# Optimization experiments

Hardware: AMD Instinct MI355X
Metric: run time of the kernel (lower is better)

## Reference

```python
import jax, jax.numpy as jnp
import numpy as np

B, S, D = 32, 1024, 256
F_, K = 256, 3
T = 8192
LN_EPS = 1e-5


def _conv1d(x, w, b, padding):
    # x: [B, S, C_in], w: [C_out, C_in, K] -> [B, S, C_out]
    y = jax.lax.conv_general_dilated(
        x.transpose(0, 2, 1), w, window_strides=(1,),
        padding=[(padding, padding)], dimension_numbers=('NCH', 'OIH', 'NCH'))
    return y.transpose(0, 2, 1) + b


def _layernorm(x, g, b):
    mu = jnp.mean(x, axis=-1, keepdims=True)
    var = jnp.mean(jnp.square(x - mu), axis=-1, keepdims=True)
    return (x - mu) * jax.lax.rsqrt(var + LN_EPS) * g + b


def setup_inputs() -> dict:
    key = jax.random.key(0)
    ks = jax.random.split(key, 8)
    sc = 0.02
    return {
        'x': jax.random.normal(ks[0], (B, S, D), dtype=jnp.float32),
        'mask': jnp.zeros((B, S), dtype=bool),
        'duration': jax.random.randint(ks[1], (B, S), 0, 8, dtype=jnp.int32),
        'max_len': T,
        'conv1_w': jax.random.normal(ks[2], (F_, D, K), dtype=jnp.float32) * sc,
        'conv1_b': jnp.zeros((F_,), dtype=jnp.float32),
        'ln1_g': jnp.ones((F_,), dtype=jnp.float32),
        'ln1_b': jnp.zeros((F_,), dtype=jnp.float32),
        'conv2_w': jax.random.normal(ks[3], (F_, F_, K), dtype=jnp.float32) * sc,
        'conv2_b': jnp.zeros((F_,), dtype=jnp.float32),
        'ln2_g': jnp.ones((F_,), dtype=jnp.float32),
        'ln2_b': jnp.zeros((F_,), dtype=jnp.float32),
        'lin_w': jax.random.normal(ks[4], (F_, 1), dtype=jnp.float32) * sc,
        'lin_b': jnp.zeros((1,), dtype=jnp.float32),
    }


def reference(x, mask, duration, max_len, conv1_w, conv1_b, ln1_g, ln1_b,
              conv2_w, conv2_b, ln2_g, ln2_b, lin_w, lin_b):
    # ---- duration predictor (eval mode: dropout = identity) ----
    h = _conv1d(x, conv1_w, conv1_b, (K - 1) // 2)
    h = _layernorm(jax.nn.relu(h), ln1_g, ln1_b)
    h = _conv1d(h, conv2_w, conv2_b, 1)
    h = _layernorm(jax.nn.relu(h), ln2_g, ln2_b)
    log_dur = (h @ lin_w + lin_b)[..., 0]  # [B, S]
    log_dur = jnp.where(mask, 0.0, log_dur)

    # ---- length regulator: repeat_interleave + pad, done as one gather ----
    dur = duration.astype(jnp.int32)
    cum = jnp.cumsum(dur, axis=1)                                   # [B, S]
    t = jnp.arange(max_len, dtype=jnp.int32)                        # [T]
    src_idx = jax.vmap(lambda c: jnp.searchsorted(c, t, side='right'))(cum)  # [B, T]
    mel_len = jnp.minimum(cum[:, -1], max_len)                      # [B]
    valid = t[None, :] < mel_len[:, None]                           # [B, T]
    src_idx = jnp.clip(src_idx, 0, x.shape[1] - 1)
    out = jnp.take_along_axis(x, src_idx[:, :, None], axis=1)       # [B, T, D]
    out = jnp.where(valid[:, :, None], out, 0.0)
    # duration_target path -> duration_rounded = duration, mel_mask stays None
    return out, log_dur, dur, mel_len
```

## Files before the change

kernel.cpp:

```cpp
#include <hip/hip_runtime.h>
#include <cstddef>

constexpr int Bb   = 32;
constexpr int Ss   = 1024;
constexpr int Dd   = 256;
constexpr int Ff   = 256;
constexpr int TMAX = 8192;
constexpr int MM   = Bb * Ss;
constexpr int KK   = 768;
constexpr int SP   = 1026;
constexpr float LN_EPS = 1e-5f;
constexpr int PIT  = 72;
constexpr int OPIT = 264;

constexpr int GEMM_BLK  = MM / 64;
constexpr int RIDER_PER = 2048;
constexpr int RIDER_F4  = 4096;

typedef __bf16 bf16x8 __attribute__((ext_vector_type(8)));
typedef __bf16 bf16x4 __attribute__((ext_vector_type(4)));
typedef float  f32x4  __attribute__((ext_vector_type(4)));

__global__ __launch_bounds__(256) void prep_k(
    const float* __restrict__ w1, const float* __restrict__ w2,
    __bf16* __restrict__ wTT1, __bf16* __restrict__ wTT2,
    const int* __restrict__ dur, float* __restrict__ dur_out,
    float* __restrict__ mel_out, int* __restrict__ idx,
    __bf16* __restrict__ xp2)
{
    __shared__ int ic[1024];
    __shared__ int sc[256];
    const int blk = blockIdx.x;
    const int tid = threadIdx.x;

    if (blk < 1536) {
        int i = blk * 256 + tid;
        const float* w = w1;
        __bf16* o = wTT1;
        int j = i;
        if (j >= Ff * KK) { j -= Ff * KK; w = w2; o = wTT2; }
        int d  = j & 255;
        int fk = j >> 8;
        int f  = fk / 3;
        int k  = fk - f * 3;
        o[(size_t)f * KK + k * 256 + d] = (__bf16)w[((size_t)(f * 256 + d)) * 3 + k];
        return;
    }
    if (blk >= 1568) {
        int j = (blk - 1568) * 256 + tid;
        int b = j >> 7;
        int r = (j >> 6) & 1;
        int d = (j & 63) * 4;
        *(bf16x4*)&xp2[((size_t)b * SP + (size_t)r * (SP - 1)) * 256 + d] =
            (bf16x4)(__bf16)0.f;
        return;
    }
    int b = blk - 1536;
    int4 d4 = ((const int4*)(dur + b * 1024))[tid];
    int l0 = d4.x, l1 = l0 + d4.y, l2 = l1 + d4.z, l3 = l2 + d4.w;
    sc[tid] = l3;
    __syncthreads();
    for (int off = 1; off < 256; off <<= 1) {
        int v = (tid >= off) ? sc[tid - off] : 0;
        __syncthreads();
        sc[tid] += v;
        __syncthreads();
    }
    int excl = sc[tid] - l3;
    ((int4*)ic)[tid] = make_int4(excl + l0, excl + l1, excl + l2, excl + l3);
    ((float4*)(dur_out + b * 1024))[tid] =
        make_float4((float)d4.x, (float)d4.y, (float)d4.z, (float)d4.w);
    if (tid == 255) mel_out[b] = (float)min(excl + l3, TMAX);
    __syncthreads();
    int mel = min(ic[1023], TMAX);
    for (int t = tid; t < TMAX; t += 256) {
        int lo = 0, hi = 1024;
        #pragma unroll
        for (int it = 0; it < 10; ++it) {
            int mid = (lo + hi) >> 1;
            if (ic[mid] <= t) lo = mid + 1; else hi = mid;
        }
        idx[b * TMAX + t] = (t < mel) ? min(lo, 1023) : -1;
    }
}

template<int MODE>
__global__ __launch_bounds__(256, 3) void gemm_fused(
    const float* __restrict__ Xf,
    const __bf16* __restrict__ Ap,
    const __bf16* __restrict__ Bw,
    const float* __restrict__ bias,
    const float* __restrict__ g, const float* __restrict__ bt,
    const float* __restrict__ lw, const float* __restrict__ lb,
    const unsigned char* __restrict__ mask,
    __bf16* __restrict__ outB, float* __restrict__ outF,
    const int* __restrict__ idx, f32x4* __restrict__ outv)
{
    __shared__ __bf16 As[64 * PIT];
    __shared__ __bf16 Bs[64 * OPIT];
    __shared__ __bf16 Bs2[256 * PIT - 64 * OPIT];

    const int tid = threadIdx.x;

    if (blockIdx.x >= GEMM_BLK) {
        int rblk = blockIdx.x - GEMM_BLK + MODE * RIDER_PER;
        size_t base = (size_t)rblk * RIDER_F4 + tid;
        int sarr[16];
        #pragma unroll
        for (int it = 0; it < 16; ++it) {
            size_t gg = base + (size_t)it * 256;
            sarr[it] = idx[gg >> 6];
        }
        f32x4 v[16];
        #pragma unroll
        for (int it = 0; it < 16; ++it) {
            size_t gg = base + (size_t)it * 256;
            int row = (int)(gg >> 6);
            int col = (int)(gg & 63);
            v[it] = (f32x4)0.f;
            if (sarr[it] >= 0) {
                int b = row >> 13;
                v[it] = ((const f32x4*)Xf)[((size_t)(b << 10) + sarr[it]) * 64 + col];
            }
        }
        #pragma unroll
        for (int it = 0; it < 16; ++it)
            __builtin_nontemporal_store(v[it], &outv[base + (size_t)it * 256]);
        return;
    }

    const int m0   = blockIdx.x * 64;
    const int bb   = m0 >> 10;
    const int s0   = m0 & 1023;
    const int wave = tid >> 6;
    const int lane = tid & 63;
    const int wn   = wave * 64;
    const int lm   = lane & 15;
    const int lk   = lane >> 4;

    __bf16* BsK = Bs;

    f32x4 acc[4][4] = {};

    for (int step = 0; step < KK / 64; ++step) {
        const int kk0  = step * 64;
        const int kblk = kk0 >> 8;
        const int d0   = kk0 & 255;

        if constexpr (MODE == 0) {
            #pragma unroll
            for (int i = 0; i < 4; ++i) {
                int c = i * 256 + tid;
                int r = c >> 4, q = c & 15;
                int sg = s0 + r + kblk - 1;
                bf16x4 o = (bf16x4)(__bf16)0.f;
                if ((unsigned)sg < 1024u) {
                    float4 v = *(const float4*)&Xf[
                        (((size_t)(bb << 10) + sg) << 8) + d0 + q * 4];
                    o[0] = (__bf16)v.x; o[1] = (__bf16)v.y;
                    o[2] = (__bf16)v.z; o[3] = (__bf16)v.w;
                }
                *(bf16x4*)&As[r * PIT + q * 4] = o;
            }
        } else {
            const __bf16* aSrc = Ap + (((size_t)(bb * SP + s0 + kblk)) << 8) + d0;
            #pragma unroll
            for (int i = 0; i < 2; ++i) {
                int c = i * 256 + tid, r = c >> 3, q = c & 7;
                *(bf16x8*)&As[r * PIT + q * 8] =
                    *(const bf16x8*)&aSrc[((size_t)r << 8) + q * 8];
            }
        }
        const __bf16* bSrc = Bw + kk0;
        #pragma unroll
        for (int i = 0; i < 8; ++i) {
            int c = i * 256 + tid, r = c >> 3, q = c & 7;
            *(bf16x8*)&BsK[r * PIT + q * 8] =
                *(const bf16x8*)&bSrc[(size_t)r * KK + q * 8];
        }
        __syncthreads();
        #pragma unroll
        for (int kc = 0; kc < 2; ++kc) {
            bf16x8 af[4], bfr[4];
            #pragma unroll
            for (int mi = 0; mi < 4; ++mi)
                af[mi] = *(const bf16x8*)&As[(mi * 16 + lm) * PIT + kc * 32 + lk * 8];
            #pragma unroll
            for (int ni = 0; ni < 4; ++ni)
                bfr[ni] = *(const bf16x8*)&BsK[(wn + ni * 16 + lm) * PIT + kc * 32 + lk * 8];
            #pragma unroll
            for (int mi = 0; mi < 4; ++mi)
                #pragma unroll
                for (int ni = 0; ni < 4; ++ni)
                    acc[mi][ni] = __builtin_amdgcn_mfma_f32_16x16x32_bf16(
                        af[mi], bfr[ni], acc[mi][ni], 0, 0, 0);
        }
        __syncthreads();
    }

    float* scrS = (float*)As;
    float* scrQ = scrS + 256;

    float s_[4][4] = {}, q_[4][4] = {};
    #pragma unroll
    for (int ni = 0; ni < 4; ++ni) {
        float bv = bias[wn + ni * 16 + lm];
        #pragma unroll
        for (int mi = 0; mi < 4; ++mi)
            #pragma unroll
            for (int r = 0; r < 4; ++r) {
                float h = fmaxf(acc[mi][ni][r] + bv, 0.f);
                acc[mi][ni][r] = h;
                s_[mi][r] += h;
                q_[mi][r] += h * h;
            }
    }
    #pragma unroll
    for (int off = 1; off < 16; off <<= 1)
        #pragma unroll
        for (int mi = 0; mi < 4; ++mi)
            #pragma unroll
            for (int r = 0; r < 4; ++r) {
                s_[mi][r] += __shfl_xor(s_[mi][r], off, 64);
                q_[mi][r] += __shfl_xor(q_[mi][r], off, 64);
            }
    if (lm == 0) {
        #pragma unroll
        for (int mi = 0; mi < 4; ++mi)
            #pragma unroll
            for (int r = 0; r < 4; ++r) {
                int row = mi * 16 + lk * 4 + r;
                scrS[wave * 64 + row] = s_[mi][r];
                scrQ[wave * 64 + row] = q_[mi][r];
            }
    }
    __syncthreads();

    float mu[4][4], rs[4][4];
    #pragma unroll
    for (int mi = 0; mi < 4; ++mi)
        #pragma unroll
        for (int r = 0; r < 4; ++r) {
            int row = mi * 16 + lk * 4 + r;
            float S = scrS[row] + scrS[64 + row] + scrS[128 + row] + scrS[192 + row];
            float Q = scrQ[row] + scrQ[64 + row] + scrQ[128 + row] + scrQ[192 + row];
            float m_ = S * (1.f / 256.f);
            float v_ = Q * (1.f / 256.f) - m_ * m_;
            mu[mi][r] = m_;
            rs[mi][r] = rsqrtf(v_ + LN_EPS);
        }

    if constexpr (MODE == 0) {
        __bf16* tile = Bs;
        #pragma unroll
        for (int ni = 0; ni < 4; ++ni) {
            int col = wn + ni * 16 + lm;
            float gv = g[col], bv2 = bt[col];
            #pragma unroll
            for (int mi = 0; mi < 4; ++mi)
                #pragma unroll
                for (int r = 0; r < 4; ++r) {
                    int row = mi * 16 + lk * 4 + r;
                    float o = (acc[mi][ni][r] - mu[mi][r]) * rs[mi][r] * gv + bv2;
                    tile[row * OPIT + col] = (__bf16)o;
                }
        }
        __syncthreads();
        size_t obase = ((size_t)(bb * SP + s0 + 1)) << 8;
        #pragma unroll
        for (int i = 0; i < 8; ++i) {
            int c = i * 256 + tid;
            int row = c >> 5, q = c & 31;
            *(bf16x8*)&outB[obase + ((size_t)row << 8) + q * 8] =
                *(bf16x8*)&tile[row * OPIT + q * 8];
        }
    } else {
        float p_[4][4] = {};
        #pragma unroll
        for (int ni = 0; ni < 4; ++ni) {
            int col = wn + ni * 16 + lm;
            float gv = g[col], bv2 = bt[col], wv = lw[col];
            #pragma unroll
            for (int mi = 0; mi < 4; ++mi)
                #pragma unroll
                for (int r = 0; r < 4; ++r) {
                    float o = (acc[mi][ni][r] - mu[mi][r]) * rs[mi][r] * gv + bv2;
                    p_[mi][r] += o * wv;
                }
        }
        #pragma unroll
        for (int off = 1; off < 16; off <<= 1)
            #pragma unroll
            for (int mi = 0; mi < 4; ++mi)
                #pragma unroll
                for (int r = 0; r < 4; ++r)
                    p_[mi][r] += __shfl_xor(p_[mi][r], off, 64);
        __syncthreads();
        if (lm == 0) {
            #pragma unroll
            for (int mi = 0; mi < 4; ++mi)
                #pragma unroll
                for (int r = 0; r < 4; ++r)
                    scrS[wave * 64 + (mi * 16 + lk * 4 + r)] = p_[mi][r];
        }
        __syncthreads();
        if (tid < 64) {
            int row = tid;
            float v = scrS[row] + scrS[64 + row] + scrS[128 + row] + scrS[192 + row]
                      + lb[0];
            if (mask[m0 + row]) v = 0.f;
            outF[m0 + row] = v;
        }
    }
}

extern "C" void kernel_launch(void* const* d_in, const int* in_sizes, int n_in,
                              void* d_out, int out_size, void* d_ws, size_t ws_size,
                              hipStream_t stream)
{
    const float* x            = (const float*)d_in[0];
    const unsigned char* mask = (const unsigned char*)d_in[1];
    const int* duration       = (const int*)d_in[2];
    const float* w1  = (const float*)d_in[4];
    const float* b1  = (const float*)d_in[5];
    const float* g1  = (const float*)d_in[6];
    const float* be1 = (const float*)d_in[7];
    const float* w2  = (const float*)d_in[8];
    const float* b2  = (const float*)d_in[9];
    const float* g2  = (const float*)d_in[10];
    const float* be2 = (const float*)d_in[11];
    const float* lw  = (const float*)d_in[12];
    const float* lb  = (const float*)d_in[13];

    float* out        = (float*)d_out;
    float* out0       = out;
    float* out_logdur = out + (size_t)Bb * TMAX * Dd;
    float* out_dur    = out_logdur + (size_t)Bb * Ss;
    float* out_mel    = out_dur + (size_t)Bb * Ss;

    char* ws = (char*)d_ws;
    __bf16* xp2  = (__bf16*)ws;
    __bf16* wTT1 = xp2 + (size_t)Bb * SP * 256;
    __bf16* wTT2 = wTT1 + (size_t)Ff * KK;
    int*    idx  = (int*)(wTT2 + (size_t)Ff * KK);

    prep_k<<<1584, 256, 0, stream>>>(w1, w2, wTT1, wTT2,
                                     duration, out_dur, out_mel, idx, xp2);
    gemm_fused<0><<<GEMM_BLK + RIDER_PER, 256, 0, stream>>>(
        x, nullptr, wTT1, b1, g1, be1, nullptr, nullptr, nullptr,
        xp2, nullptr, idx, (f32x4*)out0);
    gemm_fused<1><<<GEMM_BLK + RIDER_PER, 256, 0, stream>>>(
        x, xp2, wTT2, b2, g2, be2, lw, lb, mask,
        nullptr, out_logdur, idx, (f32x4*)out0);
}
```

Baseline: 356.2 us.

## Stage GEMM tiles via direct global-to-LDS loads with XOR-swizzled layouts

The GEMM tile loads now use global_load_lds (buffer-to-LDS DMA), which skips the register round-trip. LDS uses an XOR-swizzled 64-wide layout in place of padded pitches to avoid bank conflicts. Weights are pre-swizzled in the prep kernel to match. The first conv input is also pre-converted to a padded bf16 buffer (xp1) in prep, so both GEMM modes share one load path. This adds an extra prep pass over x and more workspace memory, in exchange for cheaper, simpler tile staging.

```diff
diff --git a/kernel.cpp b/kernel.cpp
--- a/kernel.cpp
+++ b/kernel.cpp
@@ -10,20 +10,31 @@
 constexpr int KK   = 768;
 constexpr int SP   = 1026;
 constexpr float LN_EPS = 1e-5f;
-constexpr int PIT  = 72;
 constexpr int OPIT = 264;
 
 constexpr int GEMM_BLK  = MM / 64;
 constexpr int RIDER_PER = 2048;
 constexpr int RIDER_F4  = 4096;
 
+constexpr int PREP_W   = 1536;
+constexpr int PREP_X   = Bb * SP * 64 / 256;
+constexpr int PREP_CUM = Bb;
+constexpr int PREP_PAD = 16;
+constexpr int PREP_TOT = PREP_W + PREP_X + PREP_CUM + PREP_PAD;
+
 typedef __bf16 bf16x8 __attribute__((ext_vector_type(8)));
 typedef __bf16 bf16x4 __attribute__((ext_vector_type(4)));
 typedef float  f32x4  __attribute__((ext_vector_type(4)));
 
+#define GLOAD_LDS16(gp, lp)                                                     \
+    __builtin_amdgcn_global_load_lds(                                           \
+        (const __attribute__((address_space(1))) void*)(gp),                    \
+        (__attribute__((address_space(3))) void*)(lp), 16, 0, 0)
+
 __global__ __launch_bounds__(256) void prep_k(
     const float* __restrict__ w1, const float* __restrict__ w2,
-    __bf16* __restrict__ wTT1, __bf16* __restrict__ wTT2,
+    __bf16* __restrict__ wTTs1, __bf16* __restrict__ wTTs2,
+    const float* __restrict__ x, __bf16* __restrict__ xp1,
     const int* __restrict__ dur, float* __restrict__ dur_out,
     float* __restrict__ mel_out, int* __restrict__ idx,
     __bf16* __restrict__ xp2)
@@ -33,21 +44,39 @@
     const int blk = blockIdx.x;
     const int tid = threadIdx.x;
 
-    if (blk < 1536) {
+    if (blk < PREP_W) {
         int i = blk * 256 + tid;
         const float* w = w1;
-        __bf16* o = wTT1;
+        __bf16* o = wTTs1;
         int j = i;
-        if (j >= Ff * KK) { j -= Ff * KK; w = w2; o = wTT2; }
-        int d  = j & 255;
-        int fk = j >> 8;
-        int f  = fk / 3;
-        int k  = fk - f * 3;
-        o[(size_t)f * KK + k * 256 + d] = (__bf16)w[((size_t)(f * 256 + d)) * 3 + k];
+        if (j >= Ff * KK) { j -= Ff * KK; w = w2; o = wTTs2; }
+        int e   = j & 7;
+        int cph = (j >> 3) & 7;
+        int r   = (j >> 6) & 255;
+        int st  = j >> 14;
+        int clog = cph ^ (r & 7);
+        int kk  = st * 64 + clog * 8 + e;
+        int k   = kk >> 8, d = kk & 255;
+        o[j] = (__bf16)w[((size_t)(r * 256 + d)) * 3 + k];
         return;
     }
-    if (blk >= 1568) {
-        int j = (blk - 1568) * 256 + tid;
+    if (blk < PREP_W + PREP_X) {
+        int i   = (blk - PREP_W) * 256 + tid;
+        int row = i >> 6;
+        int d4  = (i & 63) * 4;
+        int b   = row / SP;
+        int j   = row - b * SP;
+        bf16x4 o = (bf16x4)(__bf16)0.f;
+        if (j != 0 && j != SP - 1) {
+            float4 v = *(const float4*)&x[(((size_t)(b << 10) + (j - 1)) << 8) + d4];
+            o[0] = (__bf16)v.x; o[1] = (__bf16)v.y;
+            o[2] = (__bf16)v.z; o[3] = (__bf16)v.w;
+        }
+        *(bf16x4*)&xp1[((size_t)row << 8) + d4] = o;
+        return;
+    }
+    if (blk >= PREP_W + PREP_X + PREP_CUM) {
+        int j = (blk - (PREP_W + PREP_X + PREP_CUM)) * 256 + tid;
         int b = j >> 7;
         int r = (j >> 6) & 1;
         int d = (j & 63) * 4;
@@ -55,7 +84,7 @@
             (bf16x4)(__bf16)0.f;
         return;
     }
-    int b = blk - 1536;
+    int b = blk - (PREP_W + PREP_X);
     int4 d4 = ((const int4*)(dur + b * 1024))[tid];
     int l0 = d4.x, l1 = l0 + d4.y, l2 = l1 + d4.z, l3 = l2 + d4.w;
     sc[tid] = l3;
@@ -88,7 +117,7 @@
 __global__ __launch_bounds__(256, 3) void gemm_fused(
     const float* __restrict__ Xf,
     const __bf16* __restrict__ Ap,
-    const __bf16* __restrict__ Bw,
+    const __bf16* __restrict__ BwS,
     const float* __restrict__ bias,
     const float* __restrict__ g, const float* __restrict__ bt,
     const float* __restrict__ lw, const float* __restrict__ lb,
@@ -96,9 +125,9 @@
     __bf16* __restrict__ outB, float* __restrict__ outF,
     const int* __restrict__ idx, f32x4* __restrict__ outv)
 {
-    __shared__ __bf16 As[64 * PIT];
-    __shared__ __bf16 Bs[64 * OPIT];
-    __shared__ __bf16 Bs2[256 * PIT - 64 * OPIT];
+    __shared__ __bf16 SMEM[64 * 64 + 256 * 64 + 1088];
+    __bf16* As = SMEM;
+    __bf16* Bs = SMEM + 4096;
 
     const int tid = threadIdx.x;
 
@@ -137,57 +166,45 @@
     const int wn   = wave * 64;
     const int lm   = lane & 15;
     const int lk   = lane >> 4;
-
-    __bf16* BsK = Bs;
+    const int l3   = lane & 7;
+    const int lr   = lane >> 3;
+
+    const int aLaneOff = lr * 256 + ((l3 ^ lr) << 3);
+    const int ch0 = lk ^ (lm & 7);
 
     f32x4 acc[4][4] = {};
 
-    for (int step = 0; step < KK / 64; ++step) {
+    const size_t aRowBase = ((size_t)(bb * SP + s0)) << 8;
+
+    for (int step = 0; step < 12; ++step) {
         const int kk0  = step * 64;
         const int kblk = kk0 >> 8;
         const int d0   = kk0 & 255;
 
-        if constexpr (MODE == 0) {
-            #pragma unroll
-            for (int i = 0; i < 4; ++i) {
-                int c = i * 256 + tid;
-                int r = c >> 4, q = c & 15;
-                int sg = s0 + r + kblk - 1;
-                bf16x4 o = (bf16x4)(__bf16)0.f;
-                if ((unsigned)sg < 1024u) {
-                    float4 v = *(const float4*)&Xf[
-                        (((size_t)(bb << 10) + sg) << 8) + d0 + q * 4];
-                    o[0] = (__bf16)v.x; o[1] = (__bf16)v.y;
-                    o[2] = (__bf16)v.z; o[3] = (__bf16)v.w;
-                }
-                *(bf16x4*)&As[r * PIT + q * 4] = o;
-            }
-        } else {
-            const __bf16* aSrc = Ap + (((size_t)(bb * SP + s0 + kblk)) << 8) + d0;
-            #pragma unroll
-            for (int i = 0; i < 2; ++i) {
-                int c = i * 256 + tid, r = c >> 3, q = c & 7;
-                *(bf16x8*)&As[r * PIT + q * 8] =
-                    *(const bf16x8*)&aSrc[((size_t)r << 8) + q * 8];
-            }
-        }
-        const __bf16* bSrc = Bw + kk0;
+        const __bf16* aSrc = Ap + aRowBase + ((size_t)kblk << 8) + d0 + aLaneOff;
+        #pragma unroll
+        for (int i = 0; i < 2; ++i) {
+            int grp = wave * 2 + i;
+            GLOAD_LDS16(aSrc + (size_t)grp * 2048, As + grp * 512);
+        }
+        const __bf16* bSrc = BwS + (size_t)step * 16384 + lane * 8;
         #pragma unroll
         for (int i = 0; i < 8; ++i) {
-            int c = i * 256 + tid, r = c >> 3, q = c & 7;
-            *(bf16x8*)&BsK[r * PIT + q * 8] =
-                *(const bf16x8*)&bSrc[(size_t)r * KK + q * 8];
-        }
-        __syncthreads();
+            int grp = wave * 8 + i;
+            GLOAD_LDS16(bSrc + (size_t)grp * 512, Bs + grp * 512);
+        }
+        __syncthreads();
+
         #pragma unroll
         for (int kc = 0; kc < 2; ++kc) {
+            const int ch = ch0 ^ (kc << 2);
             bf16x8 af[4], bfr[4];
             #pragma unroll
             for (int mi = 0; mi < 4; ++mi)
-                af[mi] = *(const bf16x8*)&As[(mi * 16 + lm) * PIT + kc * 32 + lk * 8];
+                af[mi] = *(const bf16x8*)&As[(mi * 16 + lm) * 64 + ch * 8];
             #pragma unroll
             for (int ni = 0; ni < 4; ++ni)
-                bfr[ni] = *(const bf16x8*)&BsK[(wn + ni * 16 + lm) * PIT + kc * 32 + lk * 8];
+                bfr[ni] = *(const bf16x8*)&Bs[(wn + ni * 16 + lm) * 64 + ch * 8];
             #pragma unroll
             for (int mi = 0; mi < 4; ++mi)
                 #pragma unroll
@@ -339,17 +356,18 @@
     float* out_mel    = out_dur + (size_t)Bb * Ss;
 
     char* ws = (char*)d_ws;
-    __bf16* xp2  = (__bf16*)ws;
-    __bf16* wTT1 = xp2 + (size_t)Bb * SP * 256;
-    __bf16* wTT2 = wTT1 + (size_t)Ff * KK;
-    int*    idx  = (int*)(wTT2 + (size_t)Ff * KK);
-
-    prep_k<<<1584, 256, 0, stream>>>(w1, w2, wTT1, wTT2,
-                                     duration, out_dur, out_mel, idx, xp2);
+    __bf16* xp1   = (__bf16*)ws;
+    __bf16* xp2   = xp1 + (size_t)Bb * SP * 256;
+    __bf16* wTTs1 = xp2 + (size_t)Bb * SP * 256;
+    __bf16* wTTs2 = wTTs1 + (size_t)Ff * KK;
+    int*    idx   = (int*)(wTTs2 + (size_t)Ff * KK);
+
+    prep_k<<<PREP_TOT, 256, 0, stream>>>(w1, w2, wTTs1, wTTs2, x, xp1,
+                                         duration, out_dur, out_mel, idx, xp2);
     gemm_fused<0><<<GEMM_BLK + RIDER_PER, 256, 0, stream>>>(
-        x, nullptr, wTT1, b1, g1, be1, nullptr, nullptr, nullptr,
+        x, xp1, wTTs1, b1, g1, be1, nullptr, nullptr, nullptr,
         xp2, nullptr, idx, (f32x4*)out0);
     gemm_fused<1><<<GEMM_BLK + RIDER_PER, 256, 0, stream>>>(
-        x, xp2, wTT2, b2, g2, be2, lw, lb, mask,
+        x, xp2, wTTs2, b2, g2, be2, lw, lb, mask,
         nullptr, out_logdur, idx, (f32x4*)out0);
 }
```

New measurement: 338.4 us. -5.0%, faster.
